# Kernel optimization log

Measured on AMD Instinct MI355X. Metric: run time of the kernel, lower is better.

The kernel has to match this reference:

```python
import jax, jax.numpy as jnp
import numpy as np

S = 2048          # sequence length (single prefill sequence)
HID = 4096        # hidden_size
NH, NKV, HD = 32, 8, 128   # q heads, kv heads, head_dim
THETA = 10000.0
SCALE = HD ** -0.5


def setup_inputs() -> dict:
    key = jax.random.key(0)
    k1, k2, k3 = jax.random.split(key, 3)
    hidden_states = jax.random.normal(k1, (S, HID), jnp.float32)
    positions = jnp.arange(S, dtype=jnp.int32)
    W_qkv = jax.random.normal(k2, (HID, (NH + 2 * NKV) * HD), jnp.float32) * 0.02
    W_o = jax.random.normal(k3, (NH * HD, HID), jnp.float32) * 0.02
    return {"hidden_states": hidden_states, "positions": positions,
            "W_qkv": W_qkv, "W_o": W_o}


def _rope(x, positions):
    # x: [T, H, HD]; neox-style RoPE (rotate halves, is_neox_style=True)
    half = HD // 2
    inv_freq = 1.0 / (THETA ** (jnp.arange(half, dtype=jnp.float32) / half))
    freqs = positions.astype(jnp.float32)[:, None] * inv_freq[None, :]  # [T, half]
    cos = jnp.cos(freqs)[:, None, :]
    sin = jnp.sin(freqs)[:, None, :]
    x1, x2 = x[..., :half], x[..., half:]
    return jnp.concatenate([x1 * cos - x2 * sin, x2 * cos + x1 * sin], axis=-1)


def reference(hidden_states, positions, W_qkv, W_o):
    # fused QKV projection then split (q_size = NH*HD, kv_size = NKV*HD)
    qkv = hidden_states @ W_qkv                      # [S, (NH+2*NKV)*HD]
    q, k, v = jnp.split(qkv, [NH * HD, NH * HD + NKV * HD], axis=1)
    q = _rope(q.reshape(S, NH, HD), positions)       # [S, NH, HD]
    k = _rope(k.reshape(S, NKV, HD), positions)      # [S, NKV, HD]
    v = v.reshape(S, NKV, HD)
    # GQA: broadcast kv heads to query heads
    rep = NH // NKV
    k = jnp.repeat(k, rep, axis=1)                   # [S, NH, HD]
    v = jnp.repeat(v, rep, axis=1)
    scores = jnp.einsum('qhd,khd->hqk', q, k) * SCALE  # [NH, S, S]
    causal = jnp.tril(jnp.ones((S, S), dtype=bool))
    scores = jnp.where(causal[None], scores, jnp.finfo(scores.dtype).min)
    attn = jax.nn.softmax(scores, axis=-1)
    out = jnp.einsum('hqk,khd->qhd', attn, v).reshape(S, NH * HD)
    return out @ W_o                                 # [S, HID]
```

## Files before the change

### kernel.cpp

```cpp
#include <hip/hip_runtime.h>
#include <math.h>
#include <stdint.h>

#define S_LEN 2048
#define HID 4096
#define NH 32
#define NKV 8
#define HD 128
#define QKV_N ((NH + 2*NKV) * HD)
#define NQK (NH + NKV)
static __device__ __constant__ const float SCALE_F = 0.08838834764831845f;

typedef __bf16 bf16x8 __attribute__((ext_vector_type(8)));
typedef __bf16 bf16x4 __attribute__((ext_vector_type(4)));
typedef float  f32x4  __attribute__((ext_vector_type(4)));
typedef uint32_t u32x4 __attribute__((ext_vector_type(4)));

#define GLD_LDS(gptr, lptr) \
  __builtin_amdgcn_global_load_lds( \
      (const __attribute__((address_space(1))) uint32_t*)(gptr), \
      (__attribute__((address_space(3))) uint32_t*)(lptr), 16, 0, 0)

__device__ __forceinline__ void tp64(const float* __restrict__ in, __bf16* __restrict__ out,
                                     int R, int C, int bx, int by, int tid, float* tile) {
  int lr = tid >> 4;
  int lc = (tid & 15) * 4;
  #pragma unroll
  for (int p = 0; p < 4; ++p) {
    int r = p * 16 + lr;
    const float4 v = *(const float4*)&in[(size_t)(by + r) * C + bx + lc];
    float* t = &tile[r * 65 + lc];
    t[0] = v.x; t[1] = v.y; t[2] = v.z; t[3] = v.w;
  }
  __syncthreads();
  int oc = tid >> 5;
  int orr = (tid & 31) * 2;
  #pragma unroll
  for (int p = 0; p < 8; ++p) {
    int c = p * 8 + oc;
    float v0 = tile[orr * 65 + c];
    float v1 = tile[(orr + 1) * 65 + c];
    __bf16 b2[2] = { (__bf16)v0, (__bf16)v1 };
    *(uint32_t*)&out[(size_t)(bx + c) * R + by + orr] = *(uint32_t*)b2;
  }
}

__global__ __launch_bounds__(256) void fused_prep_kernel(const float* __restrict__ hidden,
                                                         __bf16* __restrict__ hid_bf,
                                                         const float* __restrict__ Wqkv,
                                                         __bf16* __restrict__ wqkvT,
                                                         const float* __restrict__ Wo,
                                                         __bf16* __restrict__ woT) {
  __shared__ float tile[64 * 65];
  const int b = blockIdx.x;
  const int tid = threadIdx.x;
  if (b < 2048) {
    const float4* in4 = (const float4*)hidden;
    int i = b * 256 + tid;
    #pragma unroll
    for (int k = 0; k < 4; ++k) {
      float4 v = in4[i + k * 524288];
      bf16x4 o = { (__bf16)v.x, (__bf16)v.y, (__bf16)v.z, (__bf16)v.w };
      *(bf16x4*)(hid_bf + (size_t)(i + k * 524288) * 4) = o;
    }
  } else if (b < 8192) {
    int id = b - 2048;
    int bx = (id % 96) * 64, by = (id / 96) * 64;
    tp64(Wqkv, wqkvT, HID, QKV_N, bx, by, tid, tile);
  } else {
    int id = b - 8192;
    int bx = (id & 63) * 64, by = (id >> 6) * 64;
    tp64(Wo, woT, HID, HID, bx, by, tid, tile);
  }
}

__global__ __launch_bounds__(256) void fused_rope_tpv_kernel(const __bf16* __restrict__ qkv,
                                                             const int* __restrict__ pos,
                                                             __bf16* __restrict__ Qr,
                                                             __bf16* __restrict__ Kr,
                                                             __bf16* __restrict__ Vt) {
  __shared__ __bf16 tile[32][33];
  const int b = blockIdx.x;
  const int tid = threadIdx.x;
  if (b < 20480) {
    int idx = b * 256 + tid;
    int half = idx & 63;
    int t = idx >> 6;
    int hh = t % NQK;
    int s = t / NQK;
    if (s >= S_LEN) return;
    float p = (float)pos[s];
    float inv_freq = exp2f((float)half * -0.2076205059304601f);
    float ang = p * inv_freq;
    float cs = cosf(ang), sn = sinf(ang);
    const __bf16* src; __bf16* dst;
    if (hh < NH) {
      src = qkv + (size_t)s * QKV_N + (size_t)hh * HD;
      dst = Qr + ((size_t)s * NH + hh) * HD;
    } else {
      int kh = hh - NH;
      src = qkv + (size_t)s * QKV_N + (size_t)NH * HD + (size_t)kh * HD;
      dst = Kr + ((size_t)s * NKV + kh) * HD;
    }
    float x1 = (float)src[half], x2 = (float)src[half + 64];
    dst[half]      = (__bf16)(x1 * cs - x2 * sn);
    dst[half + 64] = (__bf16)(x2 * cs + x1 * sn);
  } else {
    int id = b - 20480;
    int sb = (id & 63) * 32;
    int db = ((id >> 6) & 3) * 32;
    int kvh = id >> 8;
    int tx = tid & 31, ty = tid >> 5;
    const __bf16* src = qkv + (size_t)(NH + NKV) * HD + (size_t)kvh * HD;
    for (int i = 0; i < 32; i += 8)
      tile[ty + i][tx] = src[(size_t)(sb + ty + i) * QKV_N + db + tx];
    __syncthreads();
    for (int i = 0; i < 32; i += 8)
      Vt[((size_t)kvh * HD + db + ty + i) * S_LEN + sb + tx] = tile[tx][ty + i];
  }
}

template <typename OutT>
__global__ __launch_bounds__(512, 2) void gemm8p_kernel(const __bf16* __restrict__ A,
                                                        const __bf16* __restrict__ Bt,
                                                        OutT* __restrict__ C0,
                                                        OutT* __restrict__ C1,
                                                        int M, int N, int Kext, int ld) {
  __shared__ __align__(16) __bf16 sA[2][2][256 * 32];
  __shared__ __align__(16) __bf16 sB[2][2][256 * 32];
  const int tid = threadIdx.x;
  const int lane = tid & 63;
  const int wave = tid >> 6;
  const int quad = lane >> 4;
  const int l16 = lane & 15;
  const int wm = (wave >> 2) * 128;
  const int wn = (wave & 3) * 64;

  const int z = blockIdx.z;
  A += (size_t)z * Kext;
  Bt += (size_t)z * Kext;
  OutT* __restrict__ C = z ? C1 : C0;

  const int nx = gridDim.x;
  size_t bm, bn;
  if (gridDim.y == 8 && (nx & 7) == 0) {
    int lin = blockIdx.y * nx + blockIdx.x;
    int j = lin >> 3, xcd = lin & 7;
    bm = (size_t)(j & 7) * 256;
    bn = (size_t)(xcd * (nx >> 3) + (j >> 3)) * 256;
  } else {
    bm = (size_t)blockIdx.y * 256;
    bn = (size_t)blockIdx.x * 256;
  }

  const int NT = Kext >> 6;
  const int rsw = (l16 >> 1) & 3;

  f32x4 acc[8][4] = {};
  bf16x8 aR[2][4], bR[2][4];

  const int row0 = tid >> 2;
  const int chL = (tid & 3) ^ ((tid >> 3) & 3);
  const uint64_t off128 = (uint64_t)128 * ld * 2;
  uint64_t aGA = (uint64_t)(uintptr_t)A + ((bm + row0) * (size_t)ld) * 2 + (size_t)chL * 16;
  uint64_t bGA = (uint64_t)(uintptr_t)Bt + ((bn + row0) * (size_t)ld) * 2 + (size_t)chL * 16;

  typedef __attribute__((address_space(3))) __bf16 lds_bf16;
  const uint32_t sAb = (uint32_t)(uintptr_t)(lds_bf16*)&sA[0][0][0];
  const uint32_t sBb = (uint32_t)(uintptr_t)(lds_bf16*)&sB[0][0][0];
  const uint32_t wlds = (uint32_t)__builtin_amdgcn_readfirstlane(wave * 1024);
  const uint32_t aBase = sAb + (uint32_t)(((wm + l16) * 32 + (quad ^ rsw) * 8) * 2);
  const uint32_t bBase = sBb + (uint32_t)(((wn + l16) * 32 + (quad ^ rsw) * 8) * 2);

#define LDSA(bf, kk) (sAb + (bf) * 32768u + (kk) * 16384u)
#define LDSB(bf, kk) (sBb + (bf) * 32768u + (kk) * 16384u)

#define STAGE_ASM(ga, ldsbase) \
  asm volatile("s_mov_b32 m0, %0\n\t" \
               "global_load_lds_dwordx4 %2, off\n\t" \
               "s_mov_b32 m0, %1\n\t" \
               "global_load_lds_dwordx4 %3, off" \
               :: "s"((ldsbase) + wlds), "s"((ldsbase) + wlds + 8192u), \
                  "v"(ga), "v"((ga) + off128) : "memory")

#define DSRD4(dst, baseaddr) do {                                                 \
    u32x4 t0_, t1_, t2_, t3_;                                                     \
    asm volatile("ds_read_b128 %0, %4\n\t"                                        \
                 "ds_read_b128 %1, %4 offset:1024\n\t"                            \
                 "ds_read_b128 %2, %4 offset:2048\n\t"                            \
                 "ds_read_b128 %3, %4 offset:3072"                                \
                 : "=&v"(t0_), "=&v"(t1_), "=&v"(t2_), "=&v"(t3_)                 \
                 : "v"(baseaddr));                                                \
    dst[0] = __builtin_bit_cast(bf16x8, t0_);                                     \
    dst[1] = __builtin_bit_cast(bf16x8, t1_);                                     \
    dst[2] = __builtin_bit_cast(bf16x8, t2_);                                     \
    dst[3] = __builtin_bit_cast(bf16x8, t3_);                                     \
  } while (0)

#define ISSUE_A(set, bf, kk, ih) DSRD4(aR[set], aBase + (bf) * 32768u + (kk) * 16384u + (ih) * 4096u)
#define ISSUE_B(set, bf, kk)     DSRD4(bR[set], bBase + (bf) * 32768u + (kk) * 16384u)

#define MFMA16(as, bs, ih) do {                                                   \
    __builtin_amdgcn_s_setprio(1);                                                \
    _Pragma("unroll")                                                             \
    for (int i_ = 0; i_ < 4; ++i_)                                                \
      _Pragma("unroll")                                                           \
      for (int j_ = 0; j_ < 4; ++j_)                                              \
        acc[(ih) * 4 + i_][j_] = __builtin_amdgcn_mfma_f32_16x16x32_bf16(         \
            aR[as][i_], bR[bs][j_], acc[(ih) * 4 + i_][j_], 0, 0, 0);             \
    __builtin_amdgcn_s_setprio(0);                                                \
    __builtin_amdgcn_sched_barrier(0);                                            \
  } while (0)

#define BAR() __builtin_amdgcn_s_barrier()
#define LGKM4() do { asm volatile("s_waitcnt lgkmcnt(4)");                        \
                     __builtin_amdgcn_sched_barrier(0); } while (0)
#define LGKM8() do { asm volatile("s_waitcnt lgkmcnt(8)");                        \
                     __builtin_amdgcn_sched_barrier(0); } while (0)
#define VMCNT4() do { asm volatile("s_waitcnt vmcnt(4)");                         \
                      __builtin_amdgcn_sched_barrier(0); } while (0)

  STAGE_ASM(aGA,        LDSA(0, 0));
  STAGE_ASM(bGA,        LDSB(0, 0));
  STAGE_ASM(aGA + 64,   LDSA(0, 1));
  STAGE_ASM(bGA + 64,   LDSB(0, 1));
  STAGE_ASM(aGA + 128,  LDSA(1, 0));
  STAGE_ASM(bGA + 128,  LDSB(1, 0));
  aGA += 192; bGA += 192;
  asm volatile("s_waitcnt vmcnt(8)");
  __builtin_amdgcn_sched_barrier(0);
  BAR();
  ISSUE_A(0, 0, 0, 0); ISSUE_B(0, 0, 0);

  for (int u = 0; u < (NT >> 1); ++u) {
    VMCNT4();
    ISSUE_A(1, 0, 0, 1);
    BAR();
    LGKM4();
    MFMA16(0, 0, 0);
    STAGE_ASM(aGA, LDSA(1, 1)); aGA += 64;
    ISSUE_A(0, 0, 1, 0); ISSUE_B(1, 0, 1);
    BAR();
    LGKM8();
    MFMA16(1, 0, 1);
    STAGE_ASM(bGA, LDSB(1, 1)); bGA += 64;
    VMCNT4();
    ISSUE_A(1, 0, 1, 1);
    BAR();
    LGKM4();
    MFMA16(0, 1, 0);
    STAGE_ASM(aGA, LDSA(0, 0)); aGA += 64;
    ISSUE_A(0, 1, 0, 0); ISSUE_B(0, 1, 0);
    BAR();
    LGKM8();
    MFMA16(1, 1, 1);
    STAGE_ASM(bGA, LDSB(0, 0)); bGA += 64;
    VMCNT4();
    ISSUE_A(1, 1, 0, 1);
    BAR();
    LGKM4();
    MFMA16(0, 0, 0);
    STAGE_ASM(aGA, LDSA(0, 1)); aGA += 64;
    ISSUE_A(0, 1, 1, 0); ISSUE_B(1, 1, 1);
    BAR();
    LGKM8();
    MFMA16(1, 0, 1);
    STAGE_ASM(bGA, LDSB(0, 1)); bGA += 64;
    VMCNT4();
    ISSUE_A(1, 1, 1, 1);
    BAR();
    LGKM4();
    MFMA16(0, 1, 0);
    STAGE_ASM(aGA, LDSA(1, 0)); aGA += 64;
    ISSUE_A(0, 0, 0, 0); ISSUE_B(0, 0, 0);
    BAR();
    LGKM8();
    MFMA16(1, 1, 1);
    STAGE_ASM(bGA, LDSB(1, 0)); bGA += 64;
  }

  asm volatile("s_waitcnt vmcnt(0) lgkmcnt(0)");
  __builtin_amdgcn_sched_barrier(0);

  #pragma unroll
  for (int i = 0; i < 8; ++i)
    #pragma unroll
    for (int j = 0; j < 4; ++j)
      #pragma unroll
      for (int r = 0; r < 4; ++r) {
        size_t row = bm + wm + i * 16 + quad * 4 + r;
        size_t col = bn + wn + j * 16 + l16;
        C[row * (size_t)N + col] = (OutT)acc[i][j][r];
      }

#undef LDSA
#undef LDSB
#undef STAGE_ASM
#undef DSRD4
#undef ISSUE_A
#undef ISSUE_B
#undef MFMA16
#undef BAR
#undef LGKM4
#undef LGKM8
#undef VMCNT4
}

__global__ __launch_bounds__(256, 2) void attn_kernel(const __bf16* __restrict__ Qr,
                                                      const __bf16* __restrict__ Kr,
                                                      const __bf16* __restrict__ Vt,
                                                      __bf16* __restrict__ O) {
  __shared__ __align__(16) char smem[73728];
  __bf16* Ps = (__bf16*)(smem + 65536);

  const int bid = blockIdx.x;
  const int h = bid & (NH - 1);
  const int qb = (S_LEN / 64 - 1) - (bid >> 5);
  const int kvh = h >> 2;
  const int tid = threadIdx.x;
  const int lane = tid & 63, wave = tid >> 6;
  const int quad = lane >> 4, l16 = lane & 15;
  const int sw = l16 & 7;
  const int q0 = qb * 64;

#define STAGE_KV(kbase, bufv) do {                                                 \
    char* kd_ = smem + (bufv) * 16384;                                             \
    char* vd_ = smem + 32768 + (bufv) * 16384;                                     \
    _Pragma("unroll")                                                              \
    for (int pass_ = 0; pass_ < 4; ++pass_) {                                      \
      int c_ = pass_ * 256 + tid;                                                  \
      int row_ = c_ >> 4, ch_ = c_ & 15;                                           \
      int chs_ = ch_ ^ (row_ & 7);                                                 \
      GLD_LDS(&Kr[(size_t)((kbase) + row_) * (NKV * HD) + (size_t)kvh * HD + chs_ * 8], \
              kd_ + c_ * 16);                                                      \
    }                                                                              \
    _Pragma("unroll")                                                              \
    for (int pass_ = 0; pass_ < 4; ++pass_) {                                      \
      int c_ = pass_ * 256 + tid;                                                  \
      int d_ = c_ >> 3, ch_ = c_ & 7;                                              \
      int chs_ = ch_ ^ (d_ & 7);                                                   \
      GLD_LDS(&Vt[((size_t)kvh * HD + d_) * S_LEN + (kbase) + chs_ * 8],           \
              vd_ + c_ * 16);                                                      \
    }                                                                              \
  } while (0)

  bf16x8 qf[4];
  {
    const __bf16* qp = Qr + (size_t)(q0 + wave * 16 + l16) * (NH * HD) + (size_t)h * HD + quad * 8;
    for (int kk = 0; kk < 4; ++kk) qf[kk] = *(const bf16x8*)(qp + kk * 32);
  }
  f32x4 oacc[8] = {};
  float m2 = -INFINITY, l_i = 0.0f;
  const float C2 = SCALE_F * 1.4426950408889634f;

  int buf = 0;
  STAGE_KV(0, 0);
  for (int kb = 0; kb <= q0; kb += 64) {
    __syncthreads();
    if (kb + 64 <= q0) STAGE_KV(kb + 64, buf ^ 1);

    const __bf16* Ks = (const __bf16*)(smem + buf * 16384);
    const __bf16* Vs = (const __bf16*)(smem + 32768 + buf * 16384);

    f32x4 sc[4] = {};
    __builtin_amdgcn_s_setprio(1);
    for (int jt = 0; jt < 4; ++jt)
      for (int kk = 0; kk < 4; ++kk) {
        bf16x8 kf = *(const bf16x8*)&Ks[(jt * 16 + l16) * 128 + ((kk * 4 + quad) ^ sw) * 8];
        sc[jt] = __builtin_amdgcn_mfma_f32_16x16x32_bf16(kf, qf[kk], sc[jt], 0, 0, 0);
      }
    __builtin_amdgcn_s_setprio(0);

    float s[16];
    for (int jt = 0; jt < 4; ++jt)
      for (int r = 0; r < 4; ++r) s[jt * 4 + r] = sc[jt][r];
    if (kb == q0) {
      int qloc = wave * 16 + l16;
      for (int jt = 0; jt < 4; ++jt)
        for (int r = 0; r < 4; ++r)
          if (jt * 16 + quad * 4 + r > qloc) s[jt * 4 + r] = -INFINITY;
    }
    float mx = s[0];
    for (int i = 1; i < 16; ++i) mx = fmaxf(mx, s[i]);
    mx = fmaxf(mx, __shfl_xor(mx, 16, 64));
    mx = fmaxf(mx, __shfl_xor(mx, 32, 64));
    float mxs = mx * C2;
    if (!__all(mxs <= m2 + 11.54f)) {
      float m2new = fmaxf(m2, mxs);
      float alpha = exp2f(m2 - m2new);
      l_i *= alpha;
      for (int dt = 0; dt < 8; ++dt) oacc[dt] *= alpha;
      m2 = m2new;
    }
    float pv[16], sum = 0.0f;
    for (int i = 0; i < 16; ++i) { pv[i] = exp2f(fmaf(s[i], C2, -m2)); sum += pv[i]; }
    sum += __shfl_xor(sum, 16, 64);
    sum += __shfl_xor(sum, 32, 64);
    l_i += sum;

    __bf16* pw = Ps + wave * 1024 + l16 * 64;
    for (int jt = 0; jt < 4; ++jt) {
      bf16x4 pk = { (__bf16)pv[jt*4+0], (__bf16)pv[jt*4+1], (__bf16)pv[jt*4+2], (__bf16)pv[jt*4+3] };
      int chunk = jt * 2 + (quad >> 1);
      *(bf16x4*)&pw[((chunk ^ sw) * 8) + (quad & 1) * 4] = pk;
    }
    __builtin_amdgcn_s_setprio(1);
    for (int half = 0; half < 2; ++half) {
      bf16x8 pf = *(const bf16x8*)&pw[((half * 4 + quad) ^ sw) * 8];
      for (int dt = 0; dt < 8; ++dt) {
        bf16x8 vf = *(const bf16x8*)&Vs[(dt * 16 + l16) * 64 + ((half * 4 + quad) ^ sw) * 8];
        oacc[dt] = __builtin_amdgcn_mfma_f32_16x16x32_bf16(vf, pf, oacc[dt], 0, 0, 0);
      }
    }
    __builtin_amdgcn_s_setprio(0);
    buf ^= 1;
  }
  __syncthreads();

#undef STAGE_KV

  float* scr = (float*)smem + wave * 2112;
  float inv = 1.0f / l_i;
  for (int dt = 0; dt < 8; ++dt) {
    f32x4 v = oacc[dt] * inv;
    *(f32x4*)&scr[l16 * 132 + dt * 16 + quad * 4] = v;
  }
  for (int it = 0; it < 4; ++it) {
    int c = it * 64 + lane;
    int row = c >> 4, ch = c & 15;
    const float* sp = &scr[row * 132 + ch * 8];
    f32x4 a = *(const f32x4*)sp;
    f32x4 b = *(const f32x4*)(sp + 4);
    bf16x8 o = { (__bf16)a[0], (__bf16)a[1], (__bf16)a[2], (__bf16)a[3],
                 (__bf16)b[0], (__bf16)b[1], (__bf16)b[2], (__bf16)b[3] };
    *(bf16x8*)&O[(size_t)(q0 + wave * 16 + row) * (NH * HD) + (size_t)h * HD + ch * 8] = o;
  }
}

extern "C" void kernel_launch(void* const* d_in, const int* in_sizes, int n_in,
                              void* d_out, int out_size, void* d_ws, size_t ws_size,
                              hipStream_t stream) {
  const float* hidden    = (const float*)d_in[0];
  const int*   positions = (const int*)d_in[1];
  const float* Wqkv      = (const float*)d_in[2];
  const float* Wo        = (const float*)d_in[3];
  float* out = (float*)d_out;

  char* p = (char*)d_ws;
  auto alloc = [&](size_t bytes) { char* r = p; p += (bytes + 255) & ~(size_t)255; return r; };
  __bf16* hid_bf = (__bf16*)alloc((size_t)S_LEN * HID * 2);
  __bf16* wqkvT  = (__bf16*)alloc((size_t)QKV_N * HID * 2);
  __bf16* woT    = (__bf16*)alloc((size_t)HID * HID * 2);
  __bf16* qkv    = (__bf16*)alloc((size_t)S_LEN * QKV_N * 2);
  __bf16* Qr     = (__bf16*)alloc((size_t)S_LEN * NH * HD * 2);
  __bf16* Kr     = (__bf16*)alloc((size_t)S_LEN * NKV * HD * 2);
  __bf16* Vt     = (__bf16*)alloc((size_t)S_LEN * NKV * HD * 2);
  __bf16* attn   = hid_bf;

  fused_prep_kernel<<<12288, 256, 0, stream>>>(hidden, hid_bf, Wqkv, wqkvT, Wo, woT);
  gemm8p_kernel<__bf16><<<dim3(QKV_N / 256, S_LEN / 256, 1), 512, 0, stream>>>(
      hid_bf, wqkvT, qkv, qkv, S_LEN, QKV_N, HID, HID);
  fused_rope_tpv_kernel<<<22528, 256, 0, stream>>>(qkv, positions, Qr, Kr, Vt);
  attn_kernel<<<NH * (S_LEN / 64), 256, 0, stream>>>(Qr, Kr, Vt, attn);
  gemm8p_kernel<float><<<dim3(HID / 256, S_LEN / 256, 1), 512, 0, stream>>>(
      attn, woT, out, out, S_LEN, HID, HID, HID);
}
```

Before: 483.9 us.

## Process two 64-row query sub-blocks per attention block to reuse K/V tiles

```diff
diff --git a/kernel.cpp b/kernel.cpp
--- a/kernel.cpp
+++ b/kernel.cpp
@@ -315,13 +315,14 @@
 
   const int bid = blockIdx.x;
   const int h = bid & (NH - 1);
-  const int qb = (S_LEN / 64 - 1) - (bid >> 5);
+  const int j = bid >> 5;
+  const int qb = (j < 8) ? (15 - j) : (j - 8);
   const int kvh = h >> 2;
   const int tid = threadIdx.x;
   const int lane = tid & 63, wave = tid >> 6;
   const int quad = lane >> 4, l16 = lane & 15;
   const int sw = l16 & 7;
-  const int q0 = qb * 64;
+  const int q0 = qb * 128;
 
 #define STAGE_KV(kbase, bufv) do {                                                 \
     char* kd_ = smem + (bufv) * 16384;                                             \
@@ -344,96 +345,149 @@
     }                                                                              \
   } while (0)
 
-  bf16x8 qf[4];
-  {
-    const __bf16* qp = Qr + (size_t)(q0 + wave * 16 + l16) * (NH * HD) + (size_t)h * HD + quad * 8;
-    for (int kk = 0; kk < 4; ++kk) qf[kk] = *(const bf16x8*)(qp + kk * 32);
-  }
-  f32x4 oacc[8] = {};
-  float m2 = -INFINITY, l_i = 0.0f;
+#define SOFTMAX_SET(scX, m2X, liX, oaccX, maskCond, pfX) do {                      \
+    float s_[16];                                                                  \
+    _Pragma("unroll")                                                              \
+    for (int jt_ = 0; jt_ < 4; ++jt_)                                              \
+      _Pragma("unroll")                                                            \
+      for (int r_ = 0; r_ < 4; ++r_) s_[jt_ * 4 + r_] = scX[jt_][r_];              \
+    if (maskCond) {                                                                \
+      int qloc_ = wave * 16 + l16;                                                 \
+      _Pragma("unroll")                                                            \
+      for (int jt_ = 0; jt_ < 4; ++jt_)                                            \
+        _Pragma("unroll")                                                          \
+        for (int r_ = 0; r_ < 4; ++r_)                                             \
+          if (jt_ * 16 + quad * 4 + r_ > qloc_) s_[jt_ * 4 + r_] = -INFINITY;      \
+    }                                                                              \
+    float mx_ = s_[0];                                                             \
+    _Pragma("unroll")                                                              \
+    for (int i_ = 1; i_ < 16; ++i_) mx_ = fmaxf(mx_, s_[i_]);                      \
+    mx_ = fmaxf(mx_, __shfl_xor(mx_, 16, 64));                                     \
+    mx_ = fmaxf(mx_, __shfl_xor(mx_, 32, 64));                                     \
+    float mxs_ = mx_ * C2;                                                         \
+    if (!__all(mxs_ <= m2X + 11.54f)) {                                            \
+      float m2n_ = fmaxf(m2X, mxs_);                                               \
+      float al_ = exp2f(m2X - m2n_);                                               \
+      liX *= al_;                                                                  \
+      _Pragma("unroll")                                                            \
+      for (int dt_ = 0; dt_ < 8; ++dt_) oaccX[dt_] *= al_;                         \
+      m2X = m2n_;                                                                  \
+    }                                                                              \
+    float sum_ = 0.0f;                                                             \
+    __bf16* pw_ = Ps + wave * 1024 + l16 * 64;                                     \
+    _Pragma("unroll")                                                              \
+    for (int jt_ = 0; jt_ < 4; ++jt_) {                                            \
+      float e0_ = exp2f(fmaf(s_[jt_*4+0], C2, -m2X));                              \
+      float e1_ = exp2f(fmaf(s_[jt_*4+1], C2, -m2X));                              \
+      float e2_ = exp2f(fmaf(s_[jt_*4+2], C2, -m2X));                              \
+      float e3_ = exp2f(fmaf(s_[jt_*4+3], C2, -m2X));                              \
+      sum_ += (e0_ + e1_) + (e2_ + e3_);                                           \
+      bf16x4 pk_ = { (__bf16)e0_, (__bf16)e1_, (__bf16)e2_, (__bf16)e3_ };         \
+      int ch_ = jt_ * 2 + (quad >> 1);                                             \
+      *(bf16x4*)&pw_[((ch_ ^ sw) * 8) + (quad & 1) * 4] = pk_;                     \
+    }                                                                              \
+    sum_ += __shfl_xor(sum_, 16, 64);                                              \
+    sum_ += __shfl_xor(sum_, 32, 64);                                              \
+    liX += sum_;                                                                   \
+    pfX[0] = *(const bf16x8*)&pw_[((quad) ^ sw) * 8];                              \
+    pfX[1] = *(const bf16x8*)&pw_[((4 + quad) ^ sw) * 8];                          \
+  } while (0)
+
+  bf16x8 qf[2][4];
+  #pragma unroll
+  for (int s2 = 0; s2 < 2; ++s2) {
+    const __bf16* qp = Qr + (size_t)(q0 + s2 * 64 + wave * 16 + l16) * (NH * HD)
+                          + (size_t)h * HD + quad * 8;
+    #pragma unroll
+    for (int kk = 0; kk < 4; ++kk) qf[s2][kk] = *(const bf16x8*)(qp + kk * 32);
+  }
+  f32x4 oacc[2][8] = {};
+  float m2[2] = { -INFINITY, -INFINITY }, l_i[2] = { 0.0f, 0.0f };
   const float C2 = SCALE_F * 1.4426950408889634f;
+  bf16x8 pf0[2], pf1[2];
 
   int buf = 0;
   STAGE_KV(0, 0);
   for (int kb = 0; kb <= q0; kb += 64) {
     __syncthreads();
-    if (kb + 64 <= q0) STAGE_KV(kb + 64, buf ^ 1);
+    STAGE_KV(kb + 64, buf ^ 1);
 
     const __bf16* Ks = (const __bf16*)(smem + buf * 16384);
     const __bf16* Vs = (const __bf16*)(smem + 32768 + buf * 16384);
 
-    f32x4 sc[4] = {};
+    f32x4 sc0[4] = {}, sc1[4] = {};
     __builtin_amdgcn_s_setprio(1);
     for (int jt = 0; jt < 4; ++jt)
       for (int kk = 0; kk < 4; ++kk) {
         bf16x8 kf = *(const bf16x8*)&Ks[(jt * 16 + l16) * 128 + ((kk * 4 + quad) ^ sw) * 8];
-        sc[jt] = __builtin_amdgcn_mfma_f32_16x16x32_bf16(kf, qf[kk], sc[jt], 0, 0, 0);
+        sc0[jt] = __builtin_amdgcn_mfma_f32_16x16x32_bf16(kf, qf[0][kk], sc0[jt], 0, 0, 0);
+        sc1[jt] = __builtin_amdgcn_mfma_f32_16x16x32_bf16(kf, qf[1][kk], sc1[jt], 0, 0, 0);
       }
     __builtin_amdgcn_s_setprio(0);
 
-    float s[16];
-    for (int jt = 0; jt < 4; ++jt)
-      for (int r = 0; r < 4; ++r) s[jt * 4 + r] = sc[jt][r];
-    if (kb == q0) {
-      int qloc = wave * 16 + l16;
-      for (int jt = 0; jt < 4; ++jt)
-        for (int r = 0; r < 4; ++r)
-          if (jt * 16 + quad * 4 + r > qloc) s[jt * 4 + r] = -INFINITY;
-    }
-    float mx = s[0];
-    for (int i = 1; i < 16; ++i) mx = fmaxf(mx, s[i]);
-    mx = fmaxf(mx, __shfl_xor(mx, 16, 64));
-    mx = fmaxf(mx, __shfl_xor(mx, 32, 64));
-    float mxs = mx * C2;
-    if (!__all(mxs <= m2 + 11.54f)) {
-      float m2new = fmaxf(m2, mxs);
-      float alpha = exp2f(m2 - m2new);
-      l_i *= alpha;
-      for (int dt = 0; dt < 8; ++dt) oacc[dt] *= alpha;
-      m2 = m2new;
-    }
-    float pv[16], sum = 0.0f;
-    for (int i = 0; i < 16; ++i) { pv[i] = exp2f(fmaf(s[i], C2, -m2)); sum += pv[i]; }
-    sum += __shfl_xor(sum, 16, 64);
-    sum += __shfl_xor(sum, 32, 64);
-    l_i += sum;
-
-    __bf16* pw = Ps + wave * 1024 + l16 * 64;
-    for (int jt = 0; jt < 4; ++jt) {
-      bf16x4 pk = { (__bf16)pv[jt*4+0], (__bf16)pv[jt*4+1], (__bf16)pv[jt*4+2], (__bf16)pv[jt*4+3] };
-      int chunk = jt * 2 + (quad >> 1);
-      *(bf16x4*)&pw[((chunk ^ sw) * 8) + (quad & 1) * 4] = pk;
-    }
+    SOFTMAX_SET(sc0, m2[0], l_i[0], oacc[0], (kb == q0), pf0);
+    SOFTMAX_SET(sc1, m2[1], l_i[1], oacc[1], false, pf1);
+
     __builtin_amdgcn_s_setprio(1);
-    for (int half = 0; half < 2; ++half) {
-      bf16x8 pf = *(const bf16x8*)&pw[((half * 4 + quad) ^ sw) * 8];
+    for (int half = 0; half < 2; ++half)
       for (int dt = 0; dt < 8; ++dt) {
         bf16x8 vf = *(const bf16x8*)&Vs[(dt * 16 + l16) * 64 + ((half * 4 + quad) ^ sw) * 8];
-        oacc[dt] = __builtin_amdgcn_mfma_f32_16x16x32_bf16(vf, pf, oacc[dt], 0, 0, 0);
+        oacc[0][dt] = __builtin_amdgcn_mfma_f32_16x16x32_bf16(vf, pf0[half], oacc[0][dt], 0, 0, 0);
+        oacc[1][dt] = __builtin_amdgcn_mfma_f32_16x16x32_bf16(vf, pf1[half], oacc[1][dt], 0, 0, 0);
       }
-    }
     __builtin_amdgcn_s_setprio(0);
     buf ^= 1;
   }
+  {
+    __syncthreads();
+    const __bf16* Ks = (const __bf16*)(smem + buf * 16384);
+    const __bf16* Vs = (const __bf16*)(smem + 32768 + buf * 16384);
+
+    f32x4 sc1[4] = {};
+    __builtin_amdgcn_s_setprio(1);
+    for (int jt = 0; jt < 4; ++jt)
+      for (int kk = 0; kk < 4; ++kk) {
+        bf16x8 kf = *(const bf16x8*)&Ks[(jt * 16 + l16) * 128 + ((kk * 4 + quad) ^ sw) * 8];
+        sc1[jt] = __builtin_amdgcn_mfma_f32_16x16x32_bf16(kf, qf[1][kk], sc1[jt], 0, 0, 0);
+      }
+    __builtin_amdgcn_s_setprio(0);
+
+    SOFTMAX_SET(sc1, m2[1], l_i[1], oacc[1], true, pf1);
+
+    __builtin_amdgcn_s_setprio(1);
+    for (int half = 0; half < 2; ++half)
+      for (int dt = 0; dt < 8; ++dt) {
+        bf16x8 vf = *(const bf16x8*)&Vs[(dt * 16 + l16) * 64 + ((half * 4 + quad) ^ sw) * 8];
+        oacc[1][dt] = __builtin_amdgcn_mfma_f32_16x16x32_bf16(vf, pf1[half], oacc[1][dt], 0, 0, 0);
+      }
+    __builtin_amdgcn_s_setprio(0);
+  }
   __syncthreads();
 
 #undef STAGE_KV
+#undef SOFTMAX_SET
 
   float* scr = (float*)smem + wave * 2112;
-  float inv = 1.0f / l_i;
-  for (int dt = 0; dt < 8; ++dt) {
-    f32x4 v = oacc[dt] * inv;
-    *(f32x4*)&scr[l16 * 132 + dt * 16 + quad * 4] = v;
-  }
-  for (int it = 0; it < 4; ++it) {
-    int c = it * 64 + lane;
-    int row = c >> 4, ch = c & 15;
-    const float* sp = &scr[row * 132 + ch * 8];
-    f32x4 a = *(const f32x4*)sp;
-    f32x4 b = *(const f32x4*)(sp + 4);
-    bf16x8 o = { (__bf16)a[0], (__bf16)a[1], (__bf16)a[2], (__bf16)a[3],
-                 (__bf16)b[0], (__bf16)b[1], (__bf16)b[2], (__bf16)b[3] };
-    *(bf16x8*)&O[(size_t)(q0 + wave * 16 + row) * (NH * HD) + (size_t)h * HD + ch * 8] = o;
+  #pragma unroll
+  for (int s2 = 0; s2 < 2; ++s2) {
+    float inv = 1.0f / l_i[s2];
+    #pragma unroll
+    for (int dt = 0; dt < 8; ++dt) {
+      f32x4 v = oacc[s2][dt] * inv;
+      *(f32x4*)&scr[l16 * 132 + dt * 16 + quad * 4] = v;
+    }
+    #pragma unroll
+    for (int it = 0; it < 4; ++it) {
+      int c = it * 64 + lane;
+      int row = c >> 4, ch = c & 15;
+      const float* sp = &scr[row * 132 + ch * 8];
+      f32x4 a = *(const f32x4*)sp;
+      f32x4 b = *(const f32x4*)(sp + 4);
+      bf16x8 o = { (__bf16)a[0], (__bf16)a[1], (__bf16)a[2], (__bf16)a[3],
+                   (__bf16)b[0], (__bf16)b[1], (__bf16)b[2], (__bf16)b[3] };
+      *(bf16x8*)&O[(size_t)(q0 + s2 * 64 + wave * 16 + row) * (NH * HD)
+                   + (size_t)h * HD + ch * 8] = o;
+    }
   }
 }
 
@@ -461,7 +515,7 @@
   gemm8p_kernel<__bf16><<<dim3(QKV_N / 256, S_LEN / 256, 1), 512, 0, stream>>>(
       hid_bf, wqkvT, qkv, qkv, S_LEN, QKV_N, HID, HID);
   fused_rope_tpv_kernel<<<22528, 256, 0, stream>>>(qkv, positions, Qr, Kr, Vt);
-  attn_kernel<<<NH * (S_LEN / 64), 256, 0, stream>>>(Qr, Kr, Vt, attn);
+  attn_kernel<<<NH * (S_LEN / 128), 256, 0, stream>>>(Qr, Kr, Vt, attn);
   gemm8p_kernel<float><<<dim3(HID / 256, S_LEN / 256, 1), 512, 0, stream>>>(
       attn, woT, out, out, S_LEN, HID, HID, HID);
 }
```

Measured after the change: 487.5 us. Within noise of the previous version (+0.8%).
